# Kernel tuning notes

Hardware: AMD Instinct MI355X
Metric: run time of the kernel (lower is better)

## Reference

```python
import jax, jax.numpy as jnp
import numpy as np

ALPHA = 0.2       # LeakyReLU negative slope
MASK_FILL = 1e-15 # value placed at non-edges before softmax (as in the original)
OUT_DIM = 64


def setup_inputs() -> dict:
    key = jax.random.key(0)
    k1, k2, k3, k4 = jax.random.split(key, 4)
    N, IN_DIM, D = 8192, 256, OUT_DIM
    h = jax.random.normal(k1, (N, IN_DIM), dtype=jnp.float32)
    # dense 0/1 adjacency (float, used only via A > 0)
    A = jax.random.randint(k2, (N, N), 0, 2).astype(jnp.float32)
    W = jax.random.normal(k3, (IN_DIM, D), dtype=jnp.float32) * (1.0 / np.sqrt(IN_DIM))
    a = jax.random.normal(k4, (2 * D,), dtype=jnp.float32) * (1.0 / np.sqrt(2 * D))
    return {"h": h, "A": A, "W": W, "a": a}


def reference(h, A, W, a):
    D = OUT_DIM
    Wh = h @ W                                   # [N, D]
    # attn([Wh_i || Wh_j]) == Wh_i . a[:D] + Wh_j . a[D:]  -- fused, avoids [N,N,2D]
    s_src = Wh @ a[:D]                           # [N]
    s_dst = Wh @ a[D:]                           # [N]
    e = jax.nn.leaky_relu(s_src[:, None] + s_dst[None, :], negative_slope=ALPHA)  # [N, N]
    attention = jnp.where(A > 0, e, MASK_FILL)
    attention = jax.nn.softmax(attention, axis=1)
    h_prime = attention @ Wh                     # [N, D]
    return jax.nn.elu(h_prime)                   # concat=True branch
```

## Files before the change

### kernel.cpp

```cpp
#include <hip/hip_runtime.h>
#include <hip/hip_bf16.h>

#define GAT_N 8192
#define GAT_K 256
#define GAT_D 64
#define GAT_ALPHA 0.2f
#define GAT_FILL 1e-15f

typedef float f32x4 __attribute__((ext_vector_type(4)));
typedef short bf16x8 __attribute__((ext_vector_type(8)));

static __device__ __forceinline__ unsigned f2bf_u(float x) {
  unsigned u = __float_as_uint(x);
  u += 0x7FFFu + ((u >> 16) & 1u);
  return u >> 16;
}

static __device__ __forceinline__ float rfl(float x) {
  return __uint_as_float(__builtin_amdgcn_readfirstlane(__float_as_uint(x)));
}

static __device__ __forceinline__ f32x4 ntload(const float* p) {
  return __builtin_nontemporal_load((const f32x4*)p);
}

__global__ __launch_bounds__(256) void k_prep(const float* __restrict__ h,
                                              const float* __restrict__ W,
                                              const float* __restrict__ av,
                                              float* __restrict__ s_src,
                                              float* __restrict__ s_dst,
                                              short* __restrict__ WhT,
                                              float* __restrict__ bmax) {
  __shared__ short T[4][64][8];
  __shared__ float wmLds[4];
  const int tid = threadIdx.x;
  const int wv = tid >> 6, lane = tid & 63;
  const int r0 = blockIdx.x * 32 + wv * 8;

  float acc[8], acc2[8];
#pragma unroll
  for (int r = 0; r < 8; ++r) { acc[r] = 0.f; acc2[r] = 0.f; }

  for (int kc = 0; kc < GAT_K; kc += 32) {
    float Wreg[32];
#pragma unroll
    for (int e = 0; e < 32; ++e) Wreg[e] = W[(size_t)(kc + e) * GAT_D + lane];
#pragma unroll
    for (int r = 0; r < 8; ++r) {
      const f32x4* h4 = (const f32x4*)(h + (size_t)(r0 + r) * GAT_K + kc);
#pragma unroll
      for (int q = 0; q < 8; ++q) {
        f32x4 hv = h4[q];
        acc[r] += hv[0] * Wreg[4 * q + 0];
        acc2[r] += hv[1] * Wreg[4 * q + 1];
        acc[r] += hv[2] * Wreg[4 * q + 2];
        acc2[r] += hv[3] * Wreg[4 * q + 3];
      }
    }
  }

  const float a_s = av[lane];
  const float a_d = av[64 + lane];
  float wmax = -3.0e38f;
#pragma unroll
  for (int r = 0; r < 8; ++r) {
    const float accf = acc[r] + acc2[r];
    T[wv][lane][r] = (short)f2bf_u(accf);
    float vs = accf * a_s, vd = accf * a_d;
#pragma unroll
    for (int off = 32; off > 0; off >>= 1) {
      vs += __shfl_xor(vs, off);
      vd += __shfl_xor(vd, off);
    }
    if (lane == 0) { s_src[r0 + r] = vs; s_dst[r0 + r] = vd; }
    wmax = fmaxf(wmax, vd);
  }
  bf16x8 vt = *(const bf16x8*)&T[wv][lane][0];
  *(bf16x8*)(WhT + (size_t)lane * GAT_N + r0) = vt;

  if (lane == 0) wmLds[wv] = wmax;
  __syncthreads();
  if (tid == 0) {
    bmax[blockIdx.x] = fmaxf(fmaxf(wmLds[0], wmLds[1]), fmaxf(wmLds[2], wmLds[3]));
  }
}

#define BM 16
#define JB 2048
#define NWAVE 8

__global__ __launch_bounds__(512, 4) void k_attn(
    const float* __restrict__ A,
    const float* __restrict__ s_src,
    const float* __restrict__ s_dst,
    const short* __restrict__ WhT,
    const float* __restrict__ bmax,
    float* __restrict__ out) {
  __shared__ char smem[65536];

  const int tid = threadIdx.x;
  const int wv = tid >> 6, lane = tid & 63;
  const int rsub = lane & 15, kg = lane >> 4;
  const int i0 = blockIdx.x * BM;

  float bm = fmaxf(fmaxf(bmax[lane], bmax[lane + 64]),
                   fmaxf(bmax[lane + 128], bmax[lane + 192]));
#pragma unroll
  for (int off = 32; off > 0; off >>= 1) bm = fmaxf(bm, __shfl_xor(bm, off));
  const float tmax = bm;

  float si_[BM], mh_[BM];
#pragma unroll
  for (int r = 0; r < BM; ++r) {
    float s = s_src[i0 + r];
    float x0 = s + tmax;
    float m = fmaxf(fmaxf(x0, GAT_ALPHA * x0), GAT_FILL);
    si_[r] = rfl(s);
    mh_[r] = rfl(m);
  }

  bf16x8 ones;
#pragma unroll
  for (int e = 0; e < 8; ++e) ones[e] = (short)0x3F80;

  f32x4 acc0 = {0.f, 0.f, 0.f, 0.f};
  f32x4 acc1 = {0.f, 0.f, 0.f, 0.f};
  f32x4 acc2 = {0.f, 0.f, 0.f, 0.f};
  f32x4 acc3 = {0.f, 0.f, 0.f, 0.f};
  f32x4 accl = {0.f, 0.f, 0.f, 0.f};

  const short* pb0 = WhT + (size_t)(0 * 16 + rsub) * GAT_N;
  const short* pb1 = WhT + (size_t)(1 * 16 + rsub) * GAT_N;
  const short* pb2 = WhT + (size_t)(2 * 16 + rsub) * GAT_N;
  const short* pb3 = WhT + (size_t)(3 * 16 + rsub) * GAT_N;

  for (int chunk = 0; chunk < GAT_N / JB; ++chunk) {
    const int jc = chunk * JB;
    const f32x4 tj = *(const f32x4*)(s_dst + jc + tid * 4);
    const float* Abase = A + (size_t)i0 * GAT_N + jc + tid * 4;

    f32x4 a_cur = ntload(Abase);
#pragma unroll
    for (int r = 0; r < BM; ++r) {
      f32x4 a_nxt;
      if (r < BM - 1) a_nxt = ntload(Abase + (size_t)(r + 1) * GAT_N);
      const float si = si_[r], mh = mh_[r];
      unsigned pk[4];
#pragma unroll
      for (int e = 0; e < 4; ++e) {
        float x = si + tj[e];
        float v = fmaxf(x, GAT_ALPHA * x);
        v = (a_cur[e] > 0.f) ? v : GAT_FILL;
        pk[e] = f2bf_u(__expf(v - mh));
      }
      uint2 w;
      w.x = pk[0] | (pk[1] << 16);
      w.y = pk[2] | (pk[3] << 16);
      *(uint2*)(&smem[(r << 12) + ((tid << 3) ^ ((r & 7) << 4))]) = w;
      a_cur = a_nxt;
    }
    __syncthreads();

#pragma unroll
    for (int kq = 0; kq < 8; ++kq) {
      const int cb = (wv << 9) + (kq << 6) + (kg << 4);
      bf16x8 af = *(const bf16x8*)(&smem[(rsub << 12) + (cb ^ ((rsub & 7) << 4))]);
      const int bcol = jc + (wv << 8) + (kq << 5) + (kg << 3);
      bf16x8 b0 = *(const bf16x8*)(pb0 + bcol);
      bf16x8 b1 = *(const bf16x8*)(pb1 + bcol);
      bf16x8 b2 = *(const bf16x8*)(pb2 + bcol);
      bf16x8 b3 = *(const bf16x8*)(pb3 + bcol);
      acc0 = __builtin_amdgcn_mfma_f32_16x16x32_bf16(af, b0, acc0, 0, 0, 0);
      acc1 = __builtin_amdgcn_mfma_f32_16x16x32_bf16(af, b1, acc1, 0, 0, 0);
      acc2 = __builtin_amdgcn_mfma_f32_16x16x32_bf16(af, b2, acc2, 0, 0, 0);
      acc3 = __builtin_amdgcn_mfma_f32_16x16x32_bf16(af, b3, acc3, 0, 0, 0);
      accl = __builtin_amdgcn_mfma_f32_16x16x32_bf16(af, ones, accl, 0, 0, 0);
    }
    __syncthreads();
  }

  float* lds_o = (float*)smem;
  float* lds_l = (float*)(smem + 32768);
#pragma unroll
  for (int r = 0; r < 4; ++r) {
    const int orow = kg * 4 + r;
    lds_o[wv * 1024 + orow * 64 + 0 * 16 + rsub] = acc0[r];
    lds_o[wv * 1024 + orow * 64 + 1 * 16 + rsub] = acc1[r];
    lds_o[wv * 1024 + orow * 64 + 2 * 16 + rsub] = acc2[r];
    lds_o[wv * 1024 + orow * 64 + 3 * 16 + rsub] = acc3[r];
    if (rsub == 0) lds_l[wv * 16 + orow] = accl[r];
  }
  __syncthreads();

  for (int idx = tid; idx < BM * GAT_D; idx += 512) {
    const int r = idx >> 6, c = idx & 63;
    float o = 0.f, ll = 0.f;
#pragma unroll
    for (int w = 0; w < NWAVE; ++w) {
      o += lds_o[w * 1024 + r * 64 + c];
      ll += lds_l[w * 16 + r];
    }
    float val = o / ll;
    out[(size_t)(i0 + r) * GAT_D + c] = (val > 0.f) ? val : (__expf(val) - 1.f);
  }
}

extern "C" void kernel_launch(void* const* d_in, const int* in_sizes, int n_in,
                              void* d_out, int out_size, void* d_ws, size_t ws_size,
                              hipStream_t stream) {
  const float* h = (const float*)d_in[0];
  const float* A = (const float*)d_in[1];
  const float* W = (const float*)d_in[2];
  const float* a = (const float*)d_in[3];
  float* out = (float*)d_out;

  const size_t need = 69632 + (size_t)GAT_D * GAT_N * 2;
  if (ws_size < need) return;
  float* bmax = (float*)d_ws;
  float* s_src = (float*)((char*)d_ws + 4096);
  float* s_dst = (float*)((char*)d_ws + 36864);
  short* WhT = (short*)((char*)d_ws + 69632);

  k_prep<<<dim3(256), dim3(256), 0, stream>>>(h, W, a, s_src, s_dst, WhT, bmax);
  k_attn<<<dim3(GAT_N / BM), dim3(512), 0, stream>>>(A, s_src, s_dst, WhT, bmax, out);
}
```

Measured before the change: 133.6 us.

## Split fused attention into staging kernel writing bf16 probabilities and a PV MFMA kernel

The fused attention kernel is split in two. A staging kernel computes the masked exponentials from A, sums the row denominators in fp32 and writes bf16 probabilities to a 128MB workspace in an MFMA fragment layout. A second kernel then reads those fragments and a pre-swizzled Wh to run the PV matmul without LDS staging. This removes the LDS round trip and barriers of the fused version, but adds a full write and re-read of an N×N bf16 matrix through global memory.

```diff
diff --git a/kernel.cpp b/kernel.cpp
--- a/kernel.cpp
+++ b/kernel.cpp
@@ -16,20 +16,12 @@
   return u >> 16;
 }
 
-static __device__ __forceinline__ float rfl(float x) {
-  return __uint_as_float(__builtin_amdgcn_readfirstlane(__float_as_uint(x)));
-}
-
-static __device__ __forceinline__ f32x4 ntload(const float* p) {
-  return __builtin_nontemporal_load((const f32x4*)p);
-}
-
 __global__ __launch_bounds__(256) void k_prep(const float* __restrict__ h,
                                               const float* __restrict__ W,
                                               const float* __restrict__ av,
                                               float* __restrict__ s_src,
                                               float* __restrict__ s_dst,
-                                              short* __restrict__ WhT,
+                                              short* __restrict__ WhT_f,
                                               float* __restrict__ bmax) {
   __shared__ short T[4][64][8];
   __shared__ float wmLds[4];
@@ -76,7 +68,12 @@
     wmax = fmaxf(wmax, vd);
   }
   bf16x8 vt = *(const bf16x8*)&T[wv][lane][0];
-  *(bf16x8*)(WhT + (size_t)lane * GAT_N + r0) = vt;
+  {
+    const int c = r0 >> 9, f = (r0 & 511) >> 5, kgr = (r0 & 31) >> 3;
+    short* dst = WhT_f + (size_t)c * 32768 + (size_t)(lane >> 4) * 8192 +
+                 f * 512 + ((lane & 15) + 16 * kgr) * 8;
+    *(bf16x8*)dst = vt;
+  }
 
   if (lane == 0) wmLds[wv] = wmax;
   __syncthreads();
@@ -85,123 +82,129 @@
   }
 }
 
-#define BM 16
-#define JB 2048
-#define NWAVE 8
-
-__global__ __launch_bounds__(512, 4) void k_attn(
-    const float* __restrict__ A,
-    const float* __restrict__ s_src,
-    const float* __restrict__ s_dst,
-    const short* __restrict__ WhT,
-    const float* __restrict__ bmax,
-    float* __restrict__ out) {
-  __shared__ char smem[65536];
+__global__ __launch_bounds__(1024) void k_stage(const float* __restrict__ A,
+                                                const float* __restrict__ s_src,
+                                                const float* __restrict__ s_dst,
+                                                const float* __restrict__ bmax,
+                                                char* __restrict__ P_t,
+                                                float* __restrict__ l_arr) {
+  const int tid = threadIdx.x;
+  const int w = tid >> 6;
+  const int tp = tid & 63;
+  const int i0 = blockIdx.x * 16;
+  const int row = i0 + w;
+
+  float bm = fmaxf(fmaxf(bmax[tp], bmax[tp + 64]),
+                   fmaxf(bmax[tp + 128], bmax[tp + 192]));
+#pragma unroll
+  for (int off = 32; off > 0; off >>= 1) bm = fmaxf(bm, __shfl_xor(bm, off));
+  const float tmax = bm;
+
+  const float sc = s_src[row];
+  const float x0 = sc + tmax;
+  const float m = fmaxf(fmaxf(x0, GAT_ALPHA * x0), GAT_FILL);
+  const float e1 = sc - m;
+  const float e2 = GAT_ALPHA * sc - m;
+  const float ccv = __expf(GAT_FILL - m);
+
+  const float* Ar = A + (size_t)row * GAT_N + tp * 8;
+  const float* tr = s_dst + tp * 8;
+  char* Pb = P_t + (size_t)blockIdx.x * 262144 + (tp >> 2) * 1024 +
+             ((w + 16 * (tp & 3)) << 4);
+
+  float lsum = 0.f;
+  for (int c = 0; c < 16; ++c) {
+    const f32x4 a0 = *(const f32x4*)(Ar + c * 512);
+    const f32x4 a1 = *(const f32x4*)(Ar + c * 512 + 4);
+    const f32x4 t0 = *(const f32x4*)(tr + c * 512);
+    const f32x4 t1 = *(const f32x4*)(tr + c * 512 + 4);
+    float p[8];
+#pragma unroll
+    for (int e = 0; e < 4; ++e) {
+      float arg = fmaxf(t0[e] + e1, fmaf(GAT_ALPHA, t0[e], e2));
+      float pe = __expf(arg);
+      p[e] = (a0[e] > 0.f) ? pe : ccv;
+    }
+#pragma unroll
+    for (int e = 0; e < 4; ++e) {
+      float arg = fmaxf(t1[e] + e1, fmaf(GAT_ALPHA, t1[e], e2));
+      float pe = __expf(arg);
+      p[4 + e] = (a1[e] > 0.f) ? pe : ccv;
+    }
+#pragma unroll
+    for (int e = 0; e < 8; ++e) lsum += p[e];
+
+    __hip_bfloat162 b0 = __float22bfloat162_rn(float2{p[0], p[1]});
+    __hip_bfloat162 b1 = __float22bfloat162_rn(float2{p[2], p[3]});
+    __hip_bfloat162 b2 = __float22bfloat162_rn(float2{p[4], p[5]});
+    __hip_bfloat162 b3 = __float22bfloat162_rn(float2{p[6], p[7]});
+    uint4 u;
+    __builtin_memcpy(&u.x, &b0, 4);
+    __builtin_memcpy(&u.y, &b1, 4);
+    __builtin_memcpy(&u.z, &b2, 4);
+    __builtin_memcpy(&u.w, &b3, 4);
+    *(uint4*)(Pb + c * 16384) = u;
+  }
+
+#pragma unroll
+  for (int off = 32; off > 0; off >>= 1) lsum += __shfl_xor(lsum, off);
+  if (tp == 0) l_arr[row] = lsum;
+}
+
+__global__ __launch_bounds__(256) void k_pv(const short* __restrict__ WhT_f,
+                                            const char* __restrict__ P_t,
+                                            const float* __restrict__ l_arr,
+                                            float* __restrict__ out) {
+  __shared__ float lds_o[4 * 16 * 65];
 
   const int tid = threadIdx.x;
   const int wv = tid >> 6, lane = tid & 63;
   const int rsub = lane & 15, kg = lane >> 4;
-  const int i0 = blockIdx.x * BM;
-
-  float bm = fmaxf(fmaxf(bmax[lane], bmax[lane + 64]),
-                   fmaxf(bmax[lane + 128], bmax[lane + 192]));
-#pragma unroll
-  for (int off = 32; off > 0; off >>= 1) bm = fmaxf(bm, __shfl_xor(bm, off));
-  const float tmax = bm;
-
-  float si_[BM], mh_[BM];
-#pragma unroll
-  for (int r = 0; r < BM; ++r) {
-    float s = s_src[i0 + r];
-    float x0 = s + tmax;
-    float m = fmaxf(fmaxf(x0, GAT_ALPHA * x0), GAT_FILL);
-    si_[r] = rfl(s);
-    mh_[r] = rfl(m);
-  }
-
-  bf16x8 ones;
-#pragma unroll
-  for (int e = 0; e < 8; ++e) ones[e] = (short)0x3F80;
+  const int i0 = blockIdx.x * 16;
 
   f32x4 acc0 = {0.f, 0.f, 0.f, 0.f};
   f32x4 acc1 = {0.f, 0.f, 0.f, 0.f};
   f32x4 acc2 = {0.f, 0.f, 0.f, 0.f};
   f32x4 acc3 = {0.f, 0.f, 0.f, 0.f};
-  f32x4 accl = {0.f, 0.f, 0.f, 0.f};
-
-  const short* pb0 = WhT + (size_t)(0 * 16 + rsub) * GAT_N;
-  const short* pb1 = WhT + (size_t)(1 * 16 + rsub) * GAT_N;
-  const short* pb2 = WhT + (size_t)(2 * 16 + rsub) * GAT_N;
-  const short* pb3 = WhT + (size_t)(3 * 16 + rsub) * GAT_N;
-
-  for (int chunk = 0; chunk < GAT_N / JB; ++chunk) {
-    const int jc = chunk * JB;
-    const f32x4 tj = *(const f32x4*)(s_dst + jc + tid * 4);
-    const float* Abase = A + (size_t)i0 * GAT_N + jc + tid * 4;
-
-    f32x4 a_cur = ntload(Abase);
-#pragma unroll
-    for (int r = 0; r < BM; ++r) {
-      f32x4 a_nxt;
-      if (r < BM - 1) a_nxt = ntload(Abase + (size_t)(r + 1) * GAT_N);
-      const float si = si_[r], mh = mh_[r];
-      unsigned pk[4];
-#pragma unroll
-      for (int e = 0; e < 4; ++e) {
-        float x = si + tj[e];
-        float v = fmaxf(x, GAT_ALPHA * x);
-        v = (a_cur[e] > 0.f) ? v : GAT_FILL;
-        pk[e] = f2bf_u(__expf(v - mh));
-      }
-      uint2 w;
-      w.x = pk[0] | (pk[1] << 16);
-      w.y = pk[2] | (pk[3] << 16);
-      *(uint2*)(&smem[(r << 12) + ((tid << 3) ^ ((r & 7) << 4))]) = w;
-      a_cur = a_nxt;
-    }
-    __syncthreads();
-
-#pragma unroll
-    for (int kq = 0; kq < 8; ++kq) {
-      const int cb = (wv << 9) + (kq << 6) + (kg << 4);
-      bf16x8 af = *(const bf16x8*)(&smem[(rsub << 12) + (cb ^ ((rsub & 7) << 4))]);
-      const int bcol = jc + (wv << 8) + (kq << 5) + (kg << 3);
-      bf16x8 b0 = *(const bf16x8*)(pb0 + bcol);
-      bf16x8 b1 = *(const bf16x8*)(pb1 + bcol);
-      bf16x8 b2 = *(const bf16x8*)(pb2 + bcol);
-      bf16x8 b3 = *(const bf16x8*)(pb3 + bcol);
-      acc0 = __builtin_amdgcn_mfma_f32_16x16x32_bf16(af, b0, acc0, 0, 0, 0);
-      acc1 = __builtin_amdgcn_mfma_f32_16x16x32_bf16(af, b1, acc1, 0, 0, 0);
-      acc2 = __builtin_amdgcn_mfma_f32_16x16x32_bf16(af, b2, acc2, 0, 0, 0);
-      acc3 = __builtin_amdgcn_mfma_f32_16x16x32_bf16(af, b3, acc3, 0, 0, 0);
-      accl = __builtin_amdgcn_mfma_f32_16x16x32_bf16(af, ones, accl, 0, 0, 0);
-    }
-    __syncthreads();
-  }
-
-  float* lds_o = (float*)smem;
-  float* lds_l = (float*)(smem + 32768);
+
+  const char* Pb = P_t + (size_t)blockIdx.x * 262144 + lane * 16;
+  const short* Wb = WhT_f + lane * 8;
+
+  for (int c = 0; c < 16; ++c) {
+    const char* Pc = Pb + c * 16384;
+    const short* Wc = Wb + (size_t)c * 32768;
+#pragma unroll
+    for (int fi = 0; fi < 4; ++fi) {
+      const int f = wv * 4 + fi;
+      bf16x8 bP = *(const bf16x8*)(Pc + f * 1024);
+      const short* Wf = Wc + f * 512;
+      bf16x8 a0 = *(const bf16x8*)(Wf + 0 * 8192);
+      bf16x8 a1 = *(const bf16x8*)(Wf + 1 * 8192);
+      bf16x8 a2 = *(const bf16x8*)(Wf + 2 * 8192);
+      bf16x8 a3 = *(const bf16x8*)(Wf + 3 * 8192);
+      acc0 = __builtin_amdgcn_mfma_f32_16x16x32_bf16(a0, bP, acc0, 0, 0, 0);
+      acc1 = __builtin_amdgcn_mfma_f32_16x16x32_bf16(a1, bP, acc1, 0, 0, 0);
+      acc2 = __builtin_amdgcn_mfma_f32_16x16x32_bf16(a2, bP, acc2, 0, 0, 0);
+      acc3 = __builtin_amdgcn_mfma_f32_16x16x32_bf16(a3, bP, acc3, 0, 0, 0);
+    }
+  }
+
 #pragma unroll
   for (int r = 0; r < 4; ++r) {
-    const int orow = kg * 4 + r;
-    lds_o[wv * 1024 + orow * 64 + 0 * 16 + rsub] = acc0[r];
-    lds_o[wv * 1024 + orow * 64 + 1 * 16 + rsub] = acc1[r];
-    lds_o[wv * 1024 + orow * 64 + 2 * 16 + rsub] = acc2[r];
-    lds_o[wv * 1024 + orow * 64 + 3 * 16 + rsub] = acc3[r];
-    if (rsub == 0) lds_l[wv * 16 + orow] = accl[r];
+    const int d = kg * 4 + r;
+    lds_o[wv * 1040 + rsub * 65 + 0 * 16 + d] = acc0[r];
+    lds_o[wv * 1040 + rsub * 65 + 1 * 16 + d] = acc1[r];
+    lds_o[wv * 1040 + rsub * 65 + 2 * 16 + d] = acc2[r];
+    lds_o[wv * 1040 + rsub * 65 + 3 * 16 + d] = acc3[r];
   }
   __syncthreads();
 
-  for (int idx = tid; idx < BM * GAT_D; idx += 512) {
-    const int r = idx >> 6, c = idx & 63;
-    float o = 0.f, ll = 0.f;
-#pragma unroll
-    for (int w = 0; w < NWAVE; ++w) {
-      o += lds_o[w * 1024 + r * 64 + c];
-      ll += lds_l[w * 16 + r];
-    }
-    float val = o / ll;
-    out[(size_t)(i0 + r) * GAT_D + c] = (val > 0.f) ? val : (__expf(val) - 1.f);
+  for (int idx = tid; idx < 16 * GAT_D; idx += 256) {
+    const int r = idx >> 6, d = idx & 63;
+    float o = lds_o[0 * 1040 + r * 65 + d] + lds_o[1 * 1040 + r * 65 + d] +
+              lds_o[2 * 1040 + r * 65 + d] + lds_o[3 * 1040 + r * 65 + d];
+    float val = o / l_arr[i0 + r];
+    out[(size_t)(i0 + r) * GAT_D + d] = (val > 0.f) ? val : (__expf(val) - 1.f);
   }
 }
 
@@ -214,13 +217,17 @@
   const float* a = (const float*)d_in[3];
   float* out = (float*)d_out;
 
-  const size_t need = 69632 + (size_t)GAT_D * GAT_N * 2;
+  const size_t need = 2097152 + (size_t)GAT_N * GAT_N * 2;
   if (ws_size < need) return;
   float* bmax = (float*)d_ws;
   float* s_src = (float*)((char*)d_ws + 4096);
   float* s_dst = (float*)((char*)d_ws + 36864);
-  short* WhT = (short*)((char*)d_ws + 69632);
-
-  k_prep<<<dim3(256), dim3(256), 0, stream>>>(h, W, a, s_src, s_dst, WhT, bmax);
-  k_attn<<<dim3(GAT_N / BM), dim3(512), 0, stream>>>(A, s_src, s_dst, WhT, bmax, out);
-}
+  short* WhT_f = (short*)((char*)d_ws + 69632);
+  float* l_arr = (float*)((char*)d_ws + 1179648);
+  char* P_t = (char*)d_ws + 2097152;
+
+  k_prep<<<dim3(256), dim3(256), 0, stream>>>(h, W, a, s_src, s_dst, WhT_f, bmax);
+  k_stage<<<dim3(GAT_N / 16), dim3(1024), 0, stream>>>(A, s_src, s_dst, bmax,
+                                                       P_t, l_arr);
+  k_pv<<<dim3(GAT_N / 16), dim3(256), 0, stream>>>(WhT_f, P_t, l_arr, out);
+}
```

After: 229.2 us. +71.5%, slower.
